# Optimization experiments

Hardware: AMD Instinct MI355X
Metric: run time of the kernel (lower is better)

Reference implementation:

```python
import jax, jax.numpy as jnp
import numpy as np

# FP4 E2M1 representable magnitudes (sign handled separately)
_FP4_GRID = np.array([0.0, 0.5, 1.0, 1.5, 2.0, 3.0, 4.0, 6.0], dtype=np.float32)
_FP4_MIDS = (_FP4_GRID[:-1] + _FP4_GRID[1:]) / 2.0  # round-to-nearest boundaries


def fp4_quant_dequant(w):
    """Per-tensor absmax-scaled round-to-nearest FP4 (E2M1) fake quantization."""
    grid = jnp.asarray(_FP4_GRID, dtype=w.dtype)
    mids = jnp.asarray(_FP4_MIDS, dtype=w.dtype)
    scale = jnp.max(jnp.abs(w)) / 6.0  # map absmax -> top FP4 level
    a = jnp.abs(w) / scale
    idx = jnp.searchsorted(mids, a)  # nearest grid index via boundary search
    return grid[idx] * jnp.sign(w) * scale


def fp4_linear(x, W, b):
    # dequantized-weight matmul + bias, as in FP4Linear
    Wq = fp4_quant_dequant(W)
    return x @ Wq.T + b


def setup_inputs() -> dict:
    key = jax.random.key(0)
    k1, k2, k3, k4, k5 = jax.random.split(key, 5)
    B, D_IN, D_H, D_OUT = 8192, 2048, 8192, 2048
    x = jax.random.normal(k1, (B, D_IN), dtype=jnp.float32)
    W1 = jax.random.normal(k2, (D_H, D_IN), dtype=jnp.float32) * 0.02
    b1 = jax.random.normal(k3, (D_H,), dtype=jnp.float32) * 0.02
    W2 = jax.random.normal(k4, (D_OUT, D_H), dtype=jnp.float32) * 0.02
    b2 = jax.random.normal(k5, (D_OUT,), dtype=jnp.float32) * 0.02
    return {"x": x, "W1": W1, "b1": b1, "W2": W2, "b2": b2}


def reference(x, W1, b1, W2, b2):
    h = jax.nn.relu(fp4_linear(x, W1, b1))  # [B, hidden]
    y = fp4_linear(h, W2, b2)                # [B, out]
    return y
```

## Files before the change

### kernel.cpp

```cpp
#include <hip/hip_runtime.h>
#include <hip/hip_bf16.h>
#include <stdint.h>

typedef __attribute__((ext_vector_type(8))) short short8;
typedef __attribute__((ext_vector_type(4))) float f32x4;

#define AS1 __attribute__((address_space(1)))
#define AS3 __attribute__((address_space(3)))

static __device__ __forceinline__ unsigned short f2bf(float f) {
    unsigned int u = __float_as_uint(f);
    u += 0x7FFFu + ((u >> 16) & 1u);
    return (unsigned short)(u >> 16);
}

__global__ void init_amax(unsigned int* amax) {
    if (threadIdx.x < 2) amax[threadIdx.x] = 0u;
}

__global__ void absmax_kernel(const float4* __restrict__ w, size_t n4,
                              unsigned int* __restrict__ out) {
    float m = 0.0f;
    size_t i = (size_t)blockIdx.x * blockDim.x + threadIdx.x;
    size_t stride = (size_t)gridDim.x * blockDim.x;
    for (; i < n4; i += stride) {
        float4 v = w[i];
        m = fmaxf(m, fmaxf(fmaxf(fabsf(v.x), fabsf(v.y)),
                           fmaxf(fabsf(v.z), fabsf(v.w))));
    }
    #pragma unroll
    for (int off = 32; off > 0; off >>= 1)
        m = fmaxf(m, __shfl_down(m, off, 64));
    __shared__ float sm[4];
    int lane = threadIdx.x & 63, wid = threadIdx.x >> 6;
    if (lane == 0) sm[wid] = m;
    __syncthreads();
    if (threadIdx.x == 0) {
        float bm = fmaxf(fmaxf(sm[0], sm[1]), fmaxf(sm[2], sm[3]));
        atomicMax(out, __float_as_uint(bm));
    }
}

static __device__ __forceinline__ unsigned short quant_one(float wv, float scale) {
    float a = fabsf(wv) / scale;
    int idx = (a > 0.25f) + (a > 0.75f) + (a > 1.25f) + (a > 1.75f)
            + (a > 2.5f)  + (a > 3.5f)  + (a > 5.0f);
    const unsigned long long lo = 0x3FC03F803F000000ull;
    const unsigned long long hi = 0x40C0408040404000ull;
    unsigned long long tab = (idx < 4) ? lo : hi;
    unsigned short mag = (unsigned short)(tab >> ((idx & 3) * 16));
    unsigned short sgn = (unsigned short)((__float_as_uint(wv) >> 16) & 0x8000u);
    return (unsigned short)(mag | sgn);
}

__global__ void quant_kernel(const float4* __restrict__ w, size_t n4,
                             const unsigned int* __restrict__ amax,
                             ushort4* __restrict__ q) {
    const float scale = __uint_as_float(*amax) / 6.0f;
    size_t i = (size_t)blockIdx.x * blockDim.x + threadIdx.x;
    size_t stride = (size_t)gridDim.x * blockDim.x;
    for (; i < n4; i += stride) {
        float4 v = w[i];
        ushort4 o;
        o.x = quant_one(v.x, scale);
        o.y = quant_one(v.y, scale);
        o.z = quant_one(v.z, scale);
        o.w = quant_one(v.w, scale);
        q[i] = o;
    }
}

__global__ void cast_bf16_kernel(const float4* __restrict__ x, size_t n4,
                                 ushort4* __restrict__ o) {
    size_t i = (size_t)blockIdx.x * blockDim.x + threadIdx.x;
    size_t stride = (size_t)gridDim.x * blockDim.x;
    for (; i < n4; i += stride) {
        float4 v = x[i];
        ushort4 r;
        r.x = f2bf(v.x); r.y = f2bf(v.y); r.z = f2bf(v.z); r.w = f2bf(v.w);
        o[i] = r;
    }
}


#define GLL(gp, dst)                                                    \
    __builtin_amdgcn_global_load_lds((const AS1 unsigned int*)(gp),     \
        (AS3 unsigned int*)(dst), 16, 0, 0)

#define STGA(gp, ldsoff)                                        \
    do {                                                        \
        GLL((gp) + goffA0, lds + (ldsoff) + tid * 16);          \
        GLL((gp) + goffA1, lds + (ldsoff) + 8192 + tid * 16);   \
    } while (0)

#define STGB(gp, ldsoff)                                        \
    do {                                                        \
        GLL((gp) + goffB0, lds + (ldsoff) + tid * 16);          \
        GLL((gp) + goffB1, lds + (ldsoff) + 8192 + tid * 16);   \
    } while (0)

#define KAB(e) ((size_t)(e) * (LAYA ? 32 : 2))
#define KBB(e) ((size_t)(e) * 2)

#define LD4(dst, base, s0)                                                    \
    do {                                                                      \
        _Pragma("unroll") for (int _i = 0; _i < 4; ++_i)                      \
            dst[_i] = *(const short8*)((base) + ((s0) + _i * 2) * 1024);      \
    } while (0)

#define MFG(AH, ARR, BRR)                                                      \
    do {                                                                       \
        _Pragma("unroll") for (int _i = 0; _i < 4; ++_i)                       \
            _Pragma("unroll") for (int _j = 0; _j < 4; ++_j)                   \
                acc[(AH) * 4 + _i][_j] =                                       \
                    __builtin_amdgcn_mfma_f32_16x16x32_bf16(                   \
                        ARR[_i], BRR[_j], acc[(AH) * 4 + _i][_j], 0, 0, 0);    \
    } while (0)

#define BAR()  __builtin_amdgcn_s_barrier()
#define PRIO(x) __builtin_amdgcn_s_setprio(x)
#define SCHB() __builtin_amdgcn_sched_barrier(0)
#define LGKM(n) do { SCHB(); asm volatile("s_waitcnt lgkmcnt(" #n ")"); SCHB(); } while (0)

#define KTILE(ldsB_, ldsA_, MA1, kA1, oA1, MORE, kNXT, oB0, oB1, oA0, VMODE)   \
    do {                                                                       \
        LD4(bE, ldsB_, 0);                                  \
        LD4(aP, ldsA_, 0);                                     \
        LD4(aQ, ldsA_, 8);                                     \
        if (MA1) STGA(pA1 + KAB(kA1), oA1);                                    \
        LGKM(4);                                \
        PRIO(1); MFG(0, aP, bE); PRIO(0);                                      \
        LD4(bO, ldsB_, 1);                                        \
        LD4(aP, ldsA_, 1);                                     \
        LGKM(8);                               \
        PRIO(1); MFG(1, aQ, bE); PRIO(0);                                      \
        LD4(aQ, ldsA_, 9);                                     \
        LGKM(4);                              \
        PRIO(1); MFG(0, aP, bO); PRIO(0);                                      \
        LGKM(0);                            \
        BAR();                                                                 \
        if (MORE) { STGB(pB0 + KBB(kNXT), oB0); STGB(pB1 + KBB(kNXT), oB1);    \
                    STGA(pA0 + KAB(kNXT), oA0); }                              \
        SCHB();                                                                \
        PRIO(1); MFG(1, aQ, bO); PRIO(0);                                      \
        if (VMODE == 2) { asm volatile("s_waitcnt vmcnt(6)"); }                \
        if (VMODE == 1) { asm volatile("s_waitcnt vmcnt(0)"); }                \
        BAR();                                                                 \
    } while (0)

template <int RELU_BF16, int LAYA>
__global__ __launch_bounds__(512, 2)
void gemm8(const char* __restrict__ A,
           const unsigned short* __restrict__ B,
           const float* __restrict__ bias,
           const unsigned int* __restrict__ amax,
           float* __restrict__ outF,
           char* __restrict__ outH,
           int M, int N, int K, int gx, int cw) {
    __shared__ __align__(16) char lds[131072];

    const int tid  = threadIdx.x;
    const int lane = tid & 63;
    const int wid  = tid >> 6;
    const int wm   = wid >> 2;
    const int wn   = wid & 3;

    const int nwg = gridDim.x;
    const int wg  = blockIdx.x;
    const int c   = wg & 7;
    const int idx = wg >> 3;
    const int nc  = nwg >> 3;
    const int cxc = gx / cw;
    const int ox  = (c % cxc) * cw;
    const int oy  = (c / cxc) * (nc / cw);
    const int bx  = ox + idx % cw;
    const int by  = oy + idx / cw;
    const int col0 = bx * 256;
    const int row0 = by * 256;

    int sp = ((lane & 15) << 6) + ((lane >> 4) << 4);
    sp ^= ((sp >> 9) & 1) << 5;

    const char* ldsA_E = lds + wm * 16384 + sp;
    const char* ldsB_E = lds + 32768 + (wn >> 1) * 16384 + (wn & 1) * 8192 + sp;
    const char* ldsA_O = ldsA_E + 65536;
    const char* ldsB_O = ldsB_E + 65536;

    int goffA0, goffA1, goffB0, goffB1;
    {
        #pragma unroll
        for (int h = 0; h < 2; ++h) {
            int o = h * 8192 + tid * 16;
            int s = o >> 10, b = o & 1023;
            b ^= ((b >> 9) & 1) << 5;
            int row = ((s >> 1) << 4) + (b >> 6);
            int k   = ((s & 1) << 5) + ((b & 63) >> 1);
            int gB  = (row * K + k) * 2;
            int gA  = LAYA ? ((row >> 4) * 262144 + (k >> 4) * 512 +
                              (row & 3) * 128 + ((row >> 2) & 3) * 32 + (k & 15) * 2)
                           : gB;
            if (h == 0) { goffA0 = gA; goffB0 = gB; }
            else        { goffA1 = gA; goffB1 = gB; }
        }
    }
    const char* pA0 = A + (LAYA ? (size_t)row0 * 16384 : (size_t)row0 * K * 2);
    const char* pA1 = A + (LAYA ? (size_t)(row0 + 128) * 16384
                                : (size_t)(row0 + 128) * K * 2);
    const char* pB0 = (const char*)B + (size_t)col0 * K * 2;
    const char* pB1 = (const char*)B + (size_t)(col0 + 128) * K * 2;

    STGB(pB0, 32768); STGB(pB1, 49152); STGA(pA0, 0); STGA(pA1, 16384);
    STGB(pB0 + KBB(64), 98304); STGB(pB1 + KBB(64), 114688);
    STGA(pA0 + KAB(64), 65536);
    asm volatile("s_waitcnt vmcnt(6)");
    BAR();

    f32x4 acc[8][4] = {};
    short8 aP[4], aQ[4], bE[4], bO[4];
    const int NIT = K >> 7;

    for (int it = 0; it < NIT - 1; ++it) {
        const int o0 = it * 128;
        KTILE(ldsB_E, ldsA_E, 1, o0 + 64, 81920,
              1, o0 + 128, 32768, 49152, 0, 2);
        KTILE(ldsB_O, ldsA_O, 1, o0 + 128, 16384,
              1, o0 + 192, 98304, 114688, 65536, 2);
    }
    {
        const int o0 = (NIT - 1) * 128;
        KTILE(ldsB_E, ldsA_E, 1, o0 + 64, 81920,
              0, 0, 0, 0, 0, 1);
        KTILE(ldsB_O, ldsA_O, 0, 0, 0,
              0, 0, 0, 0, 0, 0);
    }

    const float scale = __uint_as_float(*amax) / 6.0f;

    if (RELU_BF16) {
        const int gbit = (lane >> 4) * 32 + (lane & 15) * 2;
        #pragma unroll
        for (int j = 0; j < 4; ++j) {
            const int col = col0 + wn * 64 + j * 16 + (lane & 15);
            const float bvv = bias[col];
            const size_t ktb = (size_t)((col0 >> 4) + wn * 4 + j) * 512;
            #pragma unroll
            for (int i = 0; i < 8; ++i) {
                const size_t rtb = (size_t)(((row0 + wm * 128) >> 4) + i) * 262144;
                #pragma unroll
                for (int r = 0; r < 4; ++r) {
                    float v = fmaxf(acc[i][j][r] * scale + bvv, 0.0f);
                    *(unsigned short*)(outH + rtb + ktb + r * 128 + gbit) = f2bf(v);
                }
            }
        }
    } else {
        #pragma unroll
        for (int p = 0; p < 2; ++p) {
            if (wm == p) {
                #pragma unroll
                for (int j = 0; j < 4; ++j) {
                    const int colb = wn * 64 + j * 16 + (lane & 15);
                    const float bvv = bias[col0 + colb];
                    #pragma unroll
                    for (int i = 0; i < 8; ++i) {
                        #pragma unroll
                        for (int r = 0; r < 4; ++r) {
                            const int row_l = i * 16 + (lane >> 4) * 4 + r;
                            const int blk = (colb >> 2) ^ (((row_l >> 2) & 3) << 2);
                            *(float*)(lds + row_l * 1024 + blk * 16 + (colb & 3) * 4)
                                = acc[i][j][r] * scale + bvv;
                        }
                    }
                }
            }
            asm volatile("s_waitcnt lgkmcnt(0)");
            BAR();
            #pragma unroll
            for (int q = 0; q < 16; ++q) {
                const int flat  = q * 8192 + tid * 16;
                const int row_l = flat >> 10;
                const int blk0  = (flat >> 4) & 63;
                const int blk   = blk0 ^ (((row_l >> 2) & 3) << 2);
                f32x4 v = *(const f32x4*)(lds + row_l * 1024 + blk * 16);
                *(f32x4*)(outF + (size_t)(row0 + p * 128 + row_l) * N
                                 + col0 + blk0 * 4) = v;
            }
            BAR();
        }
    }
}

extern "C" void kernel_launch(void* const* d_in, const int* in_sizes, int n_in,
                              void* d_out, int out_size, void* d_ws, size_t ws_size,
                              hipStream_t stream) {
    const float* x  = (const float*)d_in[0];
    const float* W1 = (const float*)d_in[1];
    const float* b1 = (const float*)d_in[2];
    const float* W2 = (const float*)d_in[3];
    const float* b2 = (const float*)d_in[4];
    float* out = (float*)d_out;

    const int Bm = 8192, Din = 2048, Dh = 8192, Dout = 2048;
    const size_t nW1 = (size_t)Dh * Din;
    const size_t nW2 = (size_t)Dout * Dh;
    const size_t nX  = (size_t)Bm * Din;
    const size_t nH  = (size_t)Bm * Dh;

    const size_t need = 256 + 2 * (nW1 + nW2 + nX + nH);
    if (ws_size < need) return;

    uint8_t* ws = (uint8_t*)d_ws;
    unsigned int*   amax = (unsigned int*)ws;
    unsigned short* Q1 = (unsigned short*)(ws + 256);
    unsigned short* Q2 = Q1 + nW1;
    unsigned short* Xb = Q2 + nW2;
    char*           H  = (char*)(Xb + nX);

    init_amax<<<1, 64, 0, stream>>>(amax);
    absmax_kernel<<<1024, 256, 0, stream>>>((const float4*)W1, nW1 / 4, amax + 0);
    absmax_kernel<<<1024, 256, 0, stream>>>((const float4*)W2, nW2 / 4, amax + 1);
    quant_kernel<<<2048, 256, 0, stream>>>((const float4*)W1, nW1 / 4, amax + 0, (ushort4*)Q1);
    quant_kernel<<<2048, 256, 0, stream>>>((const float4*)W2, nW2 / 4, amax + 1, (ushort4*)Q2);
    cast_bf16_kernel<<<2048, 256, 0, stream>>>((const float4*)x, nX / 4, (ushort4*)Xb);

    gemm8<1, 0><<<dim3((Dh / 256) * (Bm / 256)), 512, 0, stream>>>(
        (const char*)Xb, Q1, b1, amax + 0, nullptr, H,
        Bm, Dh, Din, Dh / 256, 16);
    gemm8<0, 1><<<dim3((Dout / 256) * (Bm / 256)), 512, 0, stream>>>(
        H, Q2, b2, amax + 1, out, nullptr,
        Bm, Dout, Dh, Dout / 256, 8);
}
```

Baseline: 534.2 us.

## Replace 256x256 8-wave GEMM with simpler 256x128 4-wave double-buffered kernel

Replaces the hand-scheduled 512-thread, 256x256-tile GEMM with a 256-thread kernel using 256x128 tiles, a K-step of 32, and a plain two-buffer LDS ping-pong. The interleaved LDS-read/MFMA schedule and the priority hints are gone, and LDS use drops to 48KB, which could allow more resident workgroups. The costs are lower arithmetic intensity per tile, a full vmcnt(0) wait and barrier on every small K-step, and more global traffic for the shared operand.

```diff
diff --git a/kernel.cpp b/kernel.cpp
--- a/kernel.cpp
+++ b/kernel.cpp
@@ -87,83 +87,56 @@
     __builtin_amdgcn_global_load_lds((const AS1 unsigned int*)(gp),     \
         (AS3 unsigned int*)(dst), 16, 0, 0)
 
-#define STGA(gp, ldsoff)                                        \
-    do {                                                        \
-        GLL((gp) + goffA0, lds + (ldsoff) + tid * 16);          \
-        GLL((gp) + goffA1, lds + (ldsoff) + 8192 + tid * 16);   \
+#define STAGE(bufw, sA, sB)                                             \
+    do {                                                                \
+        GLL(pA + (sA) + goffA0, lds + (bufw) + tid * 16);               \
+        GLL(pA + (sA) + goffA1, lds + (bufw) + 4096 + tid * 16);        \
+        GLL(pA + (sA) + goffA2, lds + (bufw) + 8192 + tid * 16);        \
+        GLL(pA + (sA) + goffA3, lds + (bufw) + 12288 + tid * 16);       \
+        GLL(pB + (sB) + goffB0, lds + (bufw) + 16384 + tid * 16);       \
+        GLL(pB + (sB) + goffB1, lds + (bufw) + 20480 + tid * 16);       \
     } while (0)
 
-#define STGB(gp, ldsoff)                                        \
-    do {                                                        \
-        GLL((gp) + goffB0, lds + (ldsoff) + tid * 16);          \
-        GLL((gp) + goffB1, lds + (ldsoff) + 8192 + tid * 16);   \
+#define RD_B(bufr)                                                      \
+    do {                                                                \
+        _Pragma("unroll") for (int _j = 0; _j < 4; ++_j)                \
+            b_[_j] = *(const short8*)(ldsB + (bufr) + _j * 1024);       \
     } while (0)
 
-#define KAB(e) ((size_t)(e) * (LAYA ? 32 : 2))
-#define KBB(e) ((size_t)(e) * 2)
-
-#define LD4(dst, base, s0)                                                    \
-    do {                                                                      \
-        _Pragma("unroll") for (int _i = 0; _i < 4; ++_i)                      \
-            dst[_i] = *(const short8*)((base) + ((s0) + _i * 2) * 1024);      \
+#define RD_A(bufr)                                                      \
+    do {                                                                \
+        _Pragma("unroll") for (int _i = 0; _i < 8; ++_i)                \
+            a_[_i] = *(const short8*)(ldsA + (bufr) + _i * 1024);       \
     } while (0)
 
-#define MFG(AH, ARR, BRR)                                                      \
+#define MF4(I0)                                                                \
     do {                                                                       \
         _Pragma("unroll") for (int _i = 0; _i < 4; ++_i)                       \
             _Pragma("unroll") for (int _j = 0; _j < 4; ++_j)                   \
-                acc[(AH) * 4 + _i][_j] =                                       \
-                    __builtin_amdgcn_mfma_f32_16x16x32_bf16(                   \
-                        ARR[_i], BRR[_j], acc[(AH) * 4 + _i][_j], 0, 0, 0);    \
+                acc[(I0) + _i][_j] = __builtin_amdgcn_mfma_f32_16x16x32_bf16(  \
+                    a_[(I0) + _i], b_[_j], acc[(I0) + _i][_j], 0, 0, 0);       \
     } while (0)
 
 #define BAR()  __builtin_amdgcn_s_barrier()
-#define PRIO(x) __builtin_amdgcn_s_setprio(x)
 #define SCHB() __builtin_amdgcn_sched_barrier(0)
 #define LGKM(n) do { SCHB(); asm volatile("s_waitcnt lgkmcnt(" #n ")"); SCHB(); } while (0)
 
-#define KTILE(ldsB_, ldsA_, MA1, kA1, oA1, MORE, kNXT, oB0, oB1, oA0, VMODE)   \
-    do {                                                                       \
-        LD4(bE, ldsB_, 0);                                  \
-        LD4(aP, ldsA_, 0);                                     \
-        LD4(aQ, ldsA_, 8);                                     \
-        if (MA1) STGA(pA1 + KAB(kA1), oA1);                                    \
-        LGKM(4);                                \
-        PRIO(1); MFG(0, aP, bE); PRIO(0);                                      \
-        LD4(bO, ldsB_, 1);                                        \
-        LD4(aP, ldsA_, 1);                                     \
-        LGKM(8);                               \
-        PRIO(1); MFG(1, aQ, bE); PRIO(0);                                      \
-        LD4(aQ, ldsA_, 9);                                     \
-        LGKM(4);                              \
-        PRIO(1); MFG(0, aP, bO); PRIO(0);                                      \
-        LGKM(0);                            \
-        BAR();                                                                 \
-        if (MORE) { STGB(pB0 + KBB(kNXT), oB0); STGB(pB1 + KBB(kNXT), oB1);    \
-                    STGA(pA0 + KAB(kNXT), oA0); }                              \
-        SCHB();                                                                \
-        PRIO(1); MFG(1, aQ, bO); PRIO(0);                                      \
-        if (VMODE == 2) { asm volatile("s_waitcnt vmcnt(6)"); }                \
-        if (VMODE == 1) { asm volatile("s_waitcnt vmcnt(0)"); }                \
-        BAR();                                                                 \
-    } while (0)
-
 template <int RELU_BF16, int LAYA>
-__global__ __launch_bounds__(512, 2)
-void gemm8(const char* __restrict__ A,
+__global__ __launch_bounds__(256, 2)
+void gemmT(const char* __restrict__ A,
            const unsigned short* __restrict__ B,
            const float* __restrict__ bias,
            const unsigned int* __restrict__ amax,
            float* __restrict__ outF,
            char* __restrict__ outH,
-           int M, int N, int K, int gx, int cw) {
-    __shared__ __align__(16) char lds[131072];
+           int N, int K, int gx, int cw, int NK) {
+    __shared__ __align__(16) char lds[49152];
 
     const int tid  = threadIdx.x;
     const int lane = tid & 63;
     const int wid  = tid >> 6;
-    const int wm   = wid >> 2;
-    const int wn   = wid & 3;
+    const int wm   = wid >> 1;
+    const int wn   = wid & 1;
 
     const int nwg = gridDim.x;
     const int wg  = blockIdx.x;
@@ -175,63 +148,71 @@
     const int oy  = (c / cxc) * (nc / cw);
     const int bx  = ox + idx % cw;
     const int by  = oy + idx / cw;
-    const int col0 = bx * 256;
+    const int col0 = bx * 128;
     const int row0 = by * 256;
 
     int sp = ((lane & 15) << 6) + ((lane >> 4) << 4);
     sp ^= ((sp >> 9) & 1) << 5;
-
-    const char* ldsA_E = lds + wm * 16384 + sp;
-    const char* ldsB_E = lds + 32768 + (wn >> 1) * 16384 + (wn & 1) * 8192 + sp;
-    const char* ldsA_O = ldsA_E + 65536;
-    const char* ldsB_O = ldsB_E + 65536;
-
-    int goffA0, goffA1, goffB0, goffB1;
+    const char* ldsA = lds + wm * 8192 + sp;
+    const char* ldsB = lds + 16384 + wn * 4096 + sp;
+
+    int goffA0, goffA1, goffA2, goffA3, goffB0, goffB1;
     {
         #pragma unroll
-        for (int h = 0; h < 2; ++h) {
-            int o = h * 8192 + tid * 16;
-            int s = o >> 10, b = o & 1023;
+        for (int j = 0; j < 4; ++j) {
+            int o = j * 4096 + tid * 16;
+            int st = o >> 10, b = o & 1023;
             b ^= ((b >> 9) & 1) << 5;
-            int row = ((s >> 1) << 4) + (b >> 6);
-            int k   = ((s & 1) << 5) + ((b & 63) >> 1);
-            int gB  = (row * K + k) * 2;
-            int gA  = LAYA ? ((row >> 4) * 262144 + (k >> 4) * 512 +
-                              (row & 3) * 128 + ((row >> 2) & 3) * 32 + (k & 15) * 2)
-                           : gB;
-            if (h == 0) { goffA0 = gA; goffB0 = gB; }
-            else        { goffA1 = gA; goffB1 = gB; }
+            int row = (st << 4) + (b >> 6);
+            int k   = (b & 63) >> 1;
+            int g = LAYA ? ((row >> 4) * 262144 + (k >> 4) * 512 +
+                            (row & 3) * 128 + ((row >> 2) & 3) * 32 + (k & 15) * 2)
+                         : (row * K + k) * 2;
+            if (j == 0) goffA0 = g; else if (j == 1) goffA1 = g;
+            else if (j == 2) goffA2 = g; else goffA3 = g;
         }
-    }
-    const char* pA0 = A + (LAYA ? (size_t)row0 * 16384 : (size_t)row0 * K * 2);
-    const char* pA1 = A + (LAYA ? (size_t)(row0 + 128) * 16384
-                                : (size_t)(row0 + 128) * K * 2);
-    const char* pB0 = (const char*)B + (size_t)col0 * K * 2;
-    const char* pB1 = (const char*)B + (size_t)(col0 + 128) * K * 2;
-
-    STGB(pB0, 32768); STGB(pB1, 49152); STGA(pA0, 0); STGA(pA1, 16384);
-    STGB(pB0 + KBB(64), 98304); STGB(pB1 + KBB(64), 114688);
-    STGA(pA0 + KAB(64), 65536);
-    asm volatile("s_waitcnt vmcnt(6)");
+        #pragma unroll
+        for (int j = 0; j < 2; ++j) {
+            int o = j * 4096 + tid * 16;
+            int st = o >> 10, b = o & 1023;
+            b ^= ((b >> 9) & 1) << 5;
+            int col = (st << 4) + (b >> 6);
+            int k   = (b & 63) >> 1;
+            int g = (col * K + k) * 2;
+            if (j == 0) goffB0 = g; else goffB1 = g;
+        }
+    }
+    const char* pA = A + (LAYA ? (size_t)(row0 >> 4) * 262144 : (size_t)row0 * K * 2);
+    const char* pB = (const char*)B + (size_t)col0 * K * 2;
+    const size_t dA = LAYA ? 1024 : 64;
+
+    STAGE(0, 0, 0);
+    asm volatile("s_waitcnt vmcnt(0)");
     BAR();
 
     f32x4 acc[8][4] = {};
-    short8 aP[4], aQ[4], bE[4], bO[4];
-    const int NIT = K >> 7;
-
-    for (int it = 0; it < NIT - 1; ++it) {
-        const int o0 = it * 128;
-        KTILE(ldsB_E, ldsA_E, 1, o0 + 64, 81920,
-              1, o0 + 128, 32768, 49152, 0, 2);
-        KTILE(ldsB_O, ldsA_O, 1, o0 + 128, 16384,
-              1, o0 + 192, 98304, 114688, 65536, 2);
+    short8 a_[8], b_[4];
+
+    for (int s = 0; s < NK - 1; ++s) {
+        const int bufr = (s & 1) * 24576;
+        const int bufw = bufr ^ 24576;
+        STAGE(bufw, (size_t)(s + 1) * dA, (size_t)(s + 1) * 64);
+        RD_B(bufr); RD_A(bufr);
+        LGKM(4);
+        MF4(0);
+        LGKM(0);
+        MF4(4);
+        asm volatile("s_waitcnt vmcnt(0)");
+        BAR();
     }
     {
-        const int o0 = (NIT - 1) * 128;
-        KTILE(ldsB_E, ldsA_E, 1, o0 + 64, 81920,
-              0, 0, 0, 0, 0, 1);
-        KTILE(ldsB_O, ldsA_O, 0, 0, 0,
-              0, 0, 0, 0, 0, 0);
+        const int bufr = ((NK - 1) & 1) * 24576;
+        RD_B(bufr); RD_A(bufr);
+        LGKM(4);
+        MF4(0);
+        LGKM(0);
+        MF4(4);
+        BAR();
     }
 
     const float scale = __uint_as_float(*amax) / 6.0f;
@@ -242,7 +223,7 @@
         for (int j = 0; j < 4; ++j) {
             const int col = col0 + wn * 64 + j * 16 + (lane & 15);
             const float bvv = bias[col];
-            const size_t ktb = (size_t)((col0 >> 4) + wn * 4 + j) * 512;
+            const size_t ktb = (size_t)(((col0 + wn * 64) >> 4) + j) * 512;
             #pragma unroll
             for (int i = 0; i < 8; ++i) {
                 const size_t rtb = (size_t)(((row0 + wm * 128) >> 4) + i) * 262144;
@@ -255,19 +236,21 @@
         }
     } else {
         #pragma unroll
-        for (int p = 0; p < 2; ++p) {
-            if (wm == p) {
+        for (int p = 0; p < 4; ++p) {
+            if (wm == (p >> 1)) {
+                const int h = p & 1;
                 #pragma unroll
                 for (int j = 0; j < 4; ++j) {
                     const int colb = wn * 64 + j * 16 + (lane & 15);
                     const float bvv = bias[col0 + colb];
                     #pragma unroll
-                    for (int i = 0; i < 8; ++i) {
+                    for (int ii = 0; ii < 4; ++ii) {
+                        const int i = h * 4 + ii;
                         #pragma unroll
                         for (int r = 0; r < 4; ++r) {
-                            const int row_l = i * 16 + (lane >> 4) * 4 + r;
+                            const int row_l = ii * 16 + (lane >> 4) * 4 + r;
                             const int blk = (colb >> 2) ^ (((row_l >> 2) & 3) << 2);
-                            *(float*)(lds + row_l * 1024 + blk * 16 + (colb & 3) * 4)
+                            *(float*)(lds + row_l * 512 + blk * 16 + (colb & 3) * 4)
                                 = acc[i][j][r] * scale + bvv;
                         }
                     }
@@ -276,13 +259,13 @@
             asm volatile("s_waitcnt lgkmcnt(0)");
             BAR();
             #pragma unroll
-            for (int q = 0; q < 16; ++q) {
-                const int flat  = q * 8192 + tid * 16;
-                const int row_l = flat >> 10;
-                const int blk0  = (flat >> 4) & 63;
+            for (int q = 0; q < 8; ++q) {
+                const int flat  = q * 4096 + tid * 16;
+                const int row_l = flat >> 9;
+                const int blk0  = (flat >> 4) & 31;
                 const int blk   = blk0 ^ (((row_l >> 2) & 3) << 2);
-                f32x4 v = *(const f32x4*)(lds + row_l * 1024 + blk * 16);
-                *(f32x4*)(outF + (size_t)(row0 + p * 128 + row_l) * N
+                f32x4 v = *(const f32x4*)(lds + row_l * 512 + blk * 16);
+                *(f32x4*)(outF + (size_t)(row0 + p * 64 + row_l) * N
                                  + col0 + blk0 * 4) = v;
             }
             BAR();
@@ -323,10 +306,10 @@
     quant_kernel<<<2048, 256, 0, stream>>>((const float4*)W2, nW2 / 4, amax + 1, (ushort4*)Q2);
     cast_bf16_kernel<<<2048, 256, 0, stream>>>((const float4*)x, nX / 4, (ushort4*)Xb);
 
-    gemm8<1, 0><<<dim3((Dh / 256) * (Bm / 256)), 512, 0, stream>>>(
+    gemmT<1, 0><<<dim3(2048), 256, 0, stream>>>(
         (const char*)Xb, Q1, b1, amax + 0, nullptr, H,
-        Bm, Dh, Din, Dh / 256, 16);
-    gemm8<0, 1><<<dim3((Dout / 256) * (Bm / 256)), 512, 0, stream>>>(
+        Dh, Din, Dh / 128, 16, Din / 32);
+    gemmT<0, 1><<<dim3(512), 256, 0, stream>>>(
         H, Q2, b2, amax + 1, out, nullptr,
-        Bm, Dout, Dh, Dout / 256, 8);
-}
+        Dout, Dh, Dout / 128, 16, Dh / 32);
+}
```

Result: slower. 565.1 us (+5.8%).
